# Optimization experiments

Measured on AMD Instinct MI355X. Metric: run time of the kernel, lower is better.

## Reference

```python
import jax, jax.numpy as jnp
import numpy as np
from jax import lax

B = 8; SEQ = 512; NVAR = 1024; PRED = 96; TFEAT = 7
DM = 128; DSTATE = 16; DCONV = 2; EL = 2; DFF = 128
DIN = DM                      # expand = 1
DTR = (DM + 15) // 16         # dt_rank = ceil(d_model/16) = 8


def setup_inputs() -> dict:
    key = jax.random.key(0)
    ks = iter(jax.random.split(key, 40))
    def rn(shape, s=0.02):
        return jax.random.normal(next(ks), shape, jnp.float32) * s
    inp = {}
    inp["x_enc"] = jax.random.normal(next(ks), (B, SEQ, NVAR), jnp.float32)
    inp["x_mark_enc"] = jax.random.normal(next(ks), (B, SEQ, TFEAT), jnp.float32)
    inp["x_dec"] = jnp.zeros((1, 1, 1), jnp.float32)
    inp["x_mark_dec"] = jnp.zeros((1, 1, 1), jnp.float32)
    # inverted embedding: Linear(seq_len -> d_model)
    inp["emb_w"] = rn((DM, SEQ)); inp["emb_b"] = jnp.zeros((DM,), jnp.float32)
    # Mamba params, stacked [e_layers, 2 directions, ...]
    inp["in_proj_w"] = rn((EL, 2, 2 * DIN, DM))
    inp["conv_w"] = rn((EL, 2, DIN, DCONV), 0.5)
    inp["conv_b"] = jnp.zeros((EL, 2, DIN), jnp.float32)
    inp["x_proj_w"] = rn((EL, 2, DTR + 2 * DSTATE, DIN))
    inp["dt_proj_w"] = rn((EL, 2, DIN, DTR), 0.5)
    inp["dt_proj_b"] = rn((EL, 2, DIN), 0.1)
    A_init = jnp.log(jnp.tile(jnp.arange(1, DSTATE + 1, dtype=jnp.float32), (DIN, 1)))
    inp["A_log"] = jnp.broadcast_to(A_init, (EL, 2, DIN, DSTATE)) * 1.0
    inp["D_param"] = jnp.ones((EL, 2, DIN), jnp.float32)
    inp["out_proj_w"] = rn((EL, 2, DM, DIN))
    # EncoderLayer norms + pointwise FFN (conv1/conv2 with kernel 1)
    inp["norm1_w"] = jnp.ones((EL, DM), jnp.float32); inp["norm1_b"] = jnp.zeros((EL, DM), jnp.float32)
    inp["norm2_w"] = jnp.ones((EL, DM), jnp.float32); inp["norm2_b"] = jnp.zeros((EL, DM), jnp.float32)
    inp["ffn_w1"] = rn((EL, DFF, DM)); inp["ffn_b1"] = jnp.zeros((EL, DFF), jnp.float32)
    inp["ffn_w2"] = rn((EL, DM, DFF)); inp["ffn_b2"] = jnp.zeros((EL, DM), jnp.float32)
    inp["fnorm_w"] = jnp.ones((DM,), jnp.float32); inp["fnorm_b"] = jnp.zeros((DM,), jnp.float32)
    inp["proj_w"] = rn((PRED, DM)); inp["proj_b"] = jnp.zeros((PRED,), jnp.float32)
    return inp


def _layernorm(x, w, b):
    mu = x.mean(-1, keepdims=True)
    var = ((x - mu) ** 2).mean(-1, keepdims=True)
    return (x - mu) / jnp.sqrt(var + 1e-5) * w + b


def _mamba(x, ipw, cw, cb, xpw, dpw, dpb, A_log, Dp, opw):
    # x: [B, L, DM]
    Bb, L, _ = x.shape
    xz = x @ ipw.T                                  # [B,L,2*DIN]
    xr, z = xz[..., :DIN], xz[..., DIN:]
    # causal depthwise conv1d, kernel DCONV, padding DCONV-1, truncated to L
    xp = jnp.pad(xr, ((0, 0), (DCONV - 1, 0), (0, 0)))
    xc = sum(xp[:, k:k + L, :] * cw[:, k] for k in range(DCONV)) + cb
    xc = jax.nn.silu(xc)
    dbc = xc @ xpw.T                                # [B,L,DTR+2*DSTATE]
    dt = dbc[..., :DTR]
    Bm = dbc[..., DTR:DTR + DSTATE]
    Cm = dbc[..., DTR + DSTATE:]
    delta = jax.nn.softplus(dt @ dpw.T + dpb)       # [B,L,DIN]
    A = -jnp.exp(A_log)                             # [DIN,DSTATE]
    dA = jnp.exp(delta[..., None] * A)              # [B,L,DIN,DSTATE]
    dBu = delta[..., None] * Bm[:, :, None, :] * xc[..., None]

    def step(h, t):
        dA_t, dBu_t, C_t = t
        h = dA_t * h + dBu_t                        # [B,DIN,DSTATE]
        y = jnp.einsum('bdn,bn->bd', h, C_t)
        return h, y

    h0 = jnp.zeros((Bb, DIN, DSTATE), x.dtype)
    _, ys = lax.scan(step, h0, (dA.transpose(1, 0, 2, 3), dBu.transpose(1, 0, 2, 3), Cm.transpose(1, 0, 2)))
    y = ys.transpose(1, 0, 2) + Dp * xc             # [B,L,DIN]
    y = y * jax.nn.silu(z)
    return y @ opw.T


def reference(x_enc, x_mark_enc, x_dec, x_mark_dec, emb_w, emb_b, in_proj_w, conv_w, conv_b,
              x_proj_w, dt_proj_w, dt_proj_b, A_log, D_param, out_proj_w,
              norm1_w, norm1_b, norm2_w, norm2_b, ffn_w1, ffn_b1, ffn_w2, ffn_b2,
              fnorm_w, fnorm_b, proj_w, proj_b):
    N = x_enc.shape[-1]
    x = jnp.where(x_enc == -9999.0, -1.0, x_enc)
    # inverted embedding: variate tokens + 7 time-feature tokens
    tokens = jnp.concatenate([x.transpose(0, 2, 1), x_mark_enc.transpose(0, 2, 1)], axis=1)  # [B,N+7,SEQ]
    h = tokens @ emb_w.T + emb_b                    # [B,N+7,DM]
    for l in range(EL):
        fwd = _mamba(h, in_proj_w[l, 0], conv_w[l, 0], conv_b[l, 0], x_proj_w[l, 0],
                     dt_proj_w[l, 0], dt_proj_b[l, 0], A_log[l, 0], D_param[l, 0], out_proj_w[l, 0])
        rev = _mamba(h[:, ::-1], in_proj_w[l, 1], conv_w[l, 1], conv_b[l, 1], x_proj_w[l, 1],
                     dt_proj_w[l, 1], dt_proj_b[l, 1], A_log[l, 1], D_param[l, 1], out_proj_w[l, 1])[:, ::-1]
        h = h + fwd + rev
        y = h = _layernorm(h, norm1_w[l], norm1_b[l])
        y = jax.nn.relu(y @ ffn_w1[l].T + ffn_b1[l])
        y = y @ ffn_w2[l].T + ffn_b2[l]
        h = _layernorm(h + y, norm2_w[l], norm2_b[l])
    h = _layernorm(h, fnorm_w, fnorm_b)
    dec = (h @ proj_w.T + proj_b).transpose(0, 2, 1)[:, :, :N]  # [B,PRED,N]
    return dec[:, -PRED:, :]
```

## Files before the change

kernel.cpp:

```cpp
#include <hip/hip_runtime.h>
#include <math.h>


#define L_SEQ 1031
#define LP    1088
#define TC    68
#define NCH   16
#define BATCH 8
#define NVAR  1024
#define SEQQ  512
#define TFEAT 7

#define SZ_H    ((size_t)BATCH * L_SEQ * 128)
#define SZ_XZ   ((size_t)2 * BATCH * L_SEQ * 256)
#define SZ_DT   ((size_t)2 * BATCH * 128 * LP)
#define SZ_BC   ((size_t)2 * BATCH * 16 * LP)
#define OFF_H    ((size_t)0)
#define OFF_H1   (OFF_H + SZ_H)
#define OFF_XZ   (OFF_H1 + SZ_H)
#define OFF_XCT  (OFF_XZ + SZ_XZ)
#define OFF_DLT  (OFF_XCT + SZ_DT)
#define OFF_BMT  (OFF_DLT + SZ_DT)
#define OFF_CMT  (OFF_BMT + SZ_BC)
#define OFF_YT   (OFF_CMT + SZ_BC)
#define SZ_SUM  ((size_t)2 * BATCH * NCH * 128 * 16)

typedef __bf16 bf16_t;
typedef bf16_t bf16x4 __attribute__((ext_vector_type(4)));
typedef bf16_t bf16x8 __attribute__((ext_vector_type(8)));
typedef float floatx4 __attribute__((ext_vector_type(4)));

#define MFMA16(a, b, c) __builtin_amdgcn_mfma_f32_16x16x32_bf16((a), (b), (c), 0, 0, 0)

__device__ __forceinline__ float silu_f(float x) {
  return x / (1.f + __expf(-x));
}
__device__ __forceinline__ float softplus_f(float x) {
  return (x > 20.f) ? x : log1pf(__expf(x));
}
__device__ __forceinline__ float red8(float x) {
  x += __int_as_float(__builtin_amdgcn_update_dpp(
      0, __float_as_int(x), 0xB1, 0xF, 0xF, true));
  x += __int_as_float(__builtin_amdgcn_update_dpp(
      0, __float_as_int(x), 0x4E, 0xF, 0xF, true));
  x += __int_as_float(__builtin_amdgcn_update_dpp(
      0, __float_as_int(x), 0x141, 0xF, 0xF, true));
  return x;
}


#define STAGE_W128(WBUF, SRC, LDK, K0)                                       \
  _Pragma("unroll")                                                          \
  for (int i_ = 0; i_ < 16; i_++) {                                          \
    int e_ = tid + i_ * 256;                                                 \
    int n_ = e_ >> 5, kq_ = e_ & 31;                                         \
    float4 wv_ = *(const float4*)&(SRC)[(size_t)n_ * (LDK) + (K0) + kq_ * 4];\
    bf16x4 bv_ = {(bf16_t)wv_.x, (bf16_t)wv_.y, (bf16_t)wv_.z, (bf16_t)wv_.w};\
    *(bf16x4*)&WBUF[n_][kq_ * 4] = bv_;                                      \
  }

#define MFMA_K128(ABUF, WBUF, ACC)                                           \
  _Pragma("unroll")                                                          \
  for (int kc_ = 0; kc_ < 4; kc_++) {                                        \
    bf16x8 a_ = *(const bf16x8*)&ABUF[arow][kc_ * 32 + q8];                  \
    _Pragma("unroll")                                                        \
    for (int nt_ = 0; nt_ < 4; nt_++) {                                      \
      bf16x8 b_ = *(const bf16x8*)&WBUF[wcol + nt_ * 16 + ln][kc_ * 32 + q8];\
      ACC[nt_] = MFMA16(a_, b_, ACC[nt_]);                                   \
    }                                                                        \
  }

__global__ __launch_bounds__(256) void k_embed(
    const float* __restrict__ x_enc, const float* __restrict__ x_mark,
    const float* __restrict__ emb_w, const float* __restrict__ emb_b,
    float* __restrict__ H) {
  int b = blockIdx.y;
  int v0 = blockIdx.x * 32;
  int tid = threadIdx.x;
  __shared__ bf16_t Abf[32][136];
  __shared__ bf16_t Wbf[128][136];
  int lane = tid & 63, ln = lane & 15, q = lane >> 4, q8 = q * 8;
  int w = tid >> 6, rw = w & 1, cw = w >> 1;
  int arow = rw * 16 + ln, wcol = cw * 64;
  floatx4 acc[4];
#pragma unroll
  for (int nt = 0; nt < 4; nt++) acc[nt] = (floatx4){0.f, 0.f, 0.f, 0.f};

  for (int c = 0; c < 4; c++) {
    int s0 = c * 128;
#pragma unroll
    for (int i = 0; i < 4; i++) {
      int e = tid + i * 256;
      int s = e >> 3, vq = e & 7;
      int vg = v0 + vq * 4;
      float4 xv;
      if (vg + 3 < NVAR) {
        xv = *(const float4*)&x_enc[((size_t)b * SEQQ + s0 + s) * NVAR + vg];
        if (xv.x == -9999.f) xv.x = -1.f;
        if (xv.y == -9999.f) xv.y = -1.f;
        if (xv.z == -9999.f) xv.z = -1.f;
        if (xv.w == -9999.f) xv.w = -1.f;
      } else {
        float tmp[4];
#pragma unroll
        for (int u = 0; u < 4; u++) {
          int v = vg + u;
          tmp[u] = (v < L_SEQ)
                       ? x_mark[((size_t)b * SEQQ + s0 + s) * TFEAT + (v - NVAR)]
                       : 0.f;
        }
        xv = make_float4(tmp[0], tmp[1], tmp[2], tmp[3]);
      }
      Abf[vq * 4 + 0][s] = (bf16_t)xv.x;
      Abf[vq * 4 + 1][s] = (bf16_t)xv.y;
      Abf[vq * 4 + 2][s] = (bf16_t)xv.z;
      Abf[vq * 4 + 3][s] = (bf16_t)xv.w;
    }
    STAGE_W128(Wbf, emb_w, SEQQ, s0);
    __syncthreads();
    MFMA_K128(Abf, Wbf, acc);
    __syncthreads();
  }
#pragma unroll
  for (int r = 0; r < 4; r++) {
    int v = v0 + rw * 16 + q * 4 + r;
    if (v < L_SEQ) {
      float* dst = &H[((size_t)b * L_SEQ + v) * 128];
#pragma unroll
      for (int nt = 0; nt < 4; nt++) {
        int col = wcol + nt * 16 + ln;
        dst[col] = acc[nt][r] + emb_b[col];
      }
    }
  }
}

__global__ __launch_bounds__(256) void k_xz(
    const float* __restrict__ H, const float* __restrict__ ipw,
    float* __restrict__ XZ, int l) {
  int b = blockIdx.y;
  int dir = blockIdx.z >> 1, nh = blockIdx.z & 1;
  int t0 = blockIdx.x * 32;
  int tid = threadIdx.x;
  __shared__ bf16_t Abf[32][136];
  __shared__ bf16_t Wbf[128][136];
  int lane = tid & 63, ln = lane & 15, q = lane >> 4, q8 = q * 8;
  int w = tid >> 6, rw = w & 1, cw = w >> 1;
  int arow = rw * 16 + ln, wcol = cw * 64;
  floatx4 acc[4];
#pragma unroll
  for (int nt = 0; nt < 4; nt++) acc[nt] = (floatx4){0.f, 0.f, 0.f, 0.f};
  const float* wbase = ipw + (size_t)(l * 2 + dir) * 256 * 128 + (size_t)nh * 128 * 128;

#pragma unroll
  for (int i = 0; i < 4; i++) {
    int e = tid + i * 256;
    int tl = e >> 5, kq = e & 31;
    int t = t0 + tl;
    float4 hv = make_float4(0.f, 0.f, 0.f, 0.f);
    if (t < L_SEQ) {
      int st = dir ? (L_SEQ - 1 - t) : t;
      hv = *(const float4*)&H[((size_t)b * L_SEQ + st) * 128 + kq * 4];
    }
    bf16x4 av = {(bf16_t)hv.x, (bf16_t)hv.y, (bf16_t)hv.z, (bf16_t)hv.w};
    *(bf16x4*)&Abf[tl][kq * 4] = av;
  }
  STAGE_W128(Wbf, wbase, 128, 0);
  __syncthreads();
  MFMA_K128(Abf, Wbf, acc);

#pragma unroll
  for (int r = 0; r < 4; r++) {
    int t = t0 + rw * 16 + q * 4 + r;
    if (t < L_SEQ) {
      float* dst = XZ + ((size_t)(dir * BATCH + b) * L_SEQ + t) * 256 + nh * 128;
#pragma unroll
      for (int nt = 0; nt < 4; nt++) dst[wcol + nt * 16 + ln] = acc[nt][r];
    }
  }
}

__global__ __launch_bounds__(256) void k_mid(
    const float* __restrict__ XZ,
    const float* __restrict__ conv_w, const float* __restrict__ conv_b,
    const float* __restrict__ xpw,
    const float* __restrict__ dpw, const float* __restrict__ dpb,
    float* __restrict__ XCT, float* __restrict__ DLT,
    float* __restrict__ BmT, float* __restrict__ CmT, int l) {
  int b = blockIdx.y, dir = blockIdx.z;
  int t0 = blockIdx.x * 32;
  int tid = threadIdx.x;
  int pg = l * 2 + dir;
  __shared__ float xcs[32][132];
  __shared__ float xpws[40][128];
  __shared__ float dbcs[40][36];
  const float* xz = XZ + (size_t)(dir * BATCH + b) * L_SEQ * 256;

  for (int i = 0; i < 20; i++) {
    int e = tid + i * 256;
    int k = e & 127, j = e >> 7;
    xpws[j][k] = xpw[((size_t)pg * 40 + j) * 128 + k];
  }
  for (int i = 0; i < 16; i++) {
    int e = tid + i * 256;
    int d = e & 127, tl = e >> 7;
    int t = t0 + tl;
    float v = 0.f;
    if (t < L_SEQ) {
      float x1 = xz[(size_t)t * 256 + d];
      float x0 = (t > 0) ? xz[(size_t)(t - 1) * 256 + d] : 0.f;
      float c0 = conv_w[((size_t)pg * 128 + d) * 2 + 0];
      float c1 = conv_w[((size_t)pg * 128 + d) * 2 + 1];
      v = silu_f(x0 * c0 + x1 * c1 + conv_b[(size_t)pg * 128 + d]);
    }
    xcs[tl][d] = v;
  }
  __syncthreads();
  {
    int tl = tid & 31, jg = tid >> 5;
    float acc[5] = {0.f};
    const float4* xrow = (const float4*)&xcs[tl][0];
    for (int kk = 0; kk < 32; kk++) {
      float4 a = xrow[kk];
#pragma unroll
      for (int jj = 0; jj < 5; jj++) {
        float4 w = ((const float4*)&xpws[jg * 5 + jj][0])[kk];
        acc[jj] = fmaf(a.x, w.x, acc[jj]);
        acc[jj] = fmaf(a.y, w.y, acc[jj]);
        acc[jj] = fmaf(a.z, w.z, acc[jj]);
        acc[jj] = fmaf(a.w, w.w, acc[jj]);
      }
    }
#pragma unroll
    for (int jj = 0; jj < 5; jj++) dbcs[jg * 5 + jj][tl] = acc[jj];
  }
  __syncthreads();
  for (int i = 0; i < 4; i++) {
    int e = tid + i * 256;
    int tl = e & 31, r = e >> 5;
    int n = r & 15, isC = r >> 4;
    int t = t0 + tl;
    if (t < LP) {
      float v = dbcs[8 + isC * 16 + n][tl];
      float* dst = isC ? CmT : BmT;
      dst[((size_t)(dir * BATCH + b) * 16 + n) * LP + t] = v;
    }
  }
  {
    int d = tid & 127, th = tid >> 7;
    float dw[8];
#pragma unroll
    for (int k = 0; k < 8; k++) dw[k] = dpw[((size_t)pg * 128 + d) * 8 + k];
    float dbv = dpb[(size_t)pg * 128 + d];
    size_t base = ((size_t)(dir * BATCH + b) * 128 + d) * LP;
    for (int tb = th * 16; tb < th * 16 + 16; tb += 4) {
      int t = t0 + tb;
      if (t < LP) {
        float dv[4], xv[4];
#pragma unroll
        for (int u = 0; u < 4; u++) {
          int tl = tb + u;
          float a = dbv;
#pragma unroll
          for (int k = 0; k < 8; k++) a = fmaf(dbcs[k][tl], dw[k], a);
          dv[u] = softplus_f(a);
          xv[u] = xcs[tl][d];
        }
        *(float4*)(DLT + base + t) = make_float4(dv[0], dv[1], dv[2], dv[3]);
        *(float4*)(XCT + base + t) = make_float4(xv[0], xv[1], xv[2], xv[3]);
      }
    }
  }
}

__global__ __launch_bounds__(64) void k_scan1(
    const float* __restrict__ DLT, const float* __restrict__ XCT,
    const float* __restrict__ BmT,
    const float* __restrict__ A_log,
    float* __restrict__ sumH, float* __restrict__ sumP, int l) {
  int z = blockIdx.z;
  int dir = z >> 4, j = z & 15;
  int b = blockIdx.y;
  int lane = threadIdx.x;
  int np = lane & 7, ds = lane >> 3;
  int d = blockIdx.x * 8 + ds;
  int pg = l * 2 + dir;
  int n0 = np * 2;
  float A0 = -__expf(A_log[((size_t)pg * 128 + d) * 16 + n0]);
  float A1 = -__expf(A_log[((size_t)pg * 128 + d) * 16 + n0 + 1]);
  size_t bd = ((size_t)(dir * BATCH + b) * 128 + d) * LP + (size_t)j * TC;
  size_t bn = ((size_t)(dir * BATCH + b) * 16 + n0) * LP + (size_t)j * TC;
  const float4* dl4 = (const float4*)(DLT + bd);
  const float4* xc4 = (const float4*)(XCT + bd);
  const float4* b04 = (const float4*)(BmT + bn);
  const float4* b14 = (const float4*)(BmT + bn + LP);
  float h0 = 0.f, h1 = 0.f, sdl = 0.f;
  const int NI = TC / 4;
  float4 cd = dl4[0], cx = xc4[0], cb0 = b04[0], cb1 = b14[0];
#define P1STEP(DL, XC, B0, B1)                       \
  {                                                  \
    float du_ = (DL) * (XC);                         \
    h0 = fmaf(__expf((DL) * A0), h0, du_ * (B0));    \
    h1 = fmaf(__expf((DL) * A1), h1, du_ * (B1));    \
  }
  for (int i = 0; i < NI; i++) {
    float4 nd = cd, nx = cx, nb0 = cb0, nb1 = cb1;
    if (i + 1 < NI) {
      nd = dl4[i + 1]; nx = xc4[i + 1];
      nb0 = b04[i + 1]; nb1 = b14[i + 1];
    }
    P1STEP(cd.x, cx.x, cb0.x, cb1.x);
    P1STEP(cd.y, cx.y, cb0.y, cb1.y);
    P1STEP(cd.z, cx.z, cb0.z, cb1.z);
    P1STEP(cd.w, cx.w, cb0.w, cb1.w);
    sdl += (cd.x + cd.y) + (cd.z + cd.w);
    cd = nd; cx = nx; cb0 = nb0; cb1 = nb1;
  }
#undef P1STEP
  size_t si = (((size_t)(dir * BATCH + b) * NCH + j) * 128 + d) * 16 + n0;
  *(float2*)&sumH[si] = make_float2(h0, h1);
  *(float2*)&sumP[si] = make_float2(__expf(A0 * sdl), __expf(A1 * sdl));
}

__global__ __launch_bounds__(64) void k_scan2(
    const float* __restrict__ DLT, const float* __restrict__ XCT,
    const float* __restrict__ BmT, const float* __restrict__ CmT,
    const float* __restrict__ XZ,
    const float* __restrict__ A_log, const float* __restrict__ Dpar,
    const float* __restrict__ sumH, const float* __restrict__ sumP,
    float* __restrict__ YT, int l) {
  int z = blockIdx.z;
  int dir = z >> 4, j = z & 15;
  int b = blockIdx.y;
  int lane = threadIdx.x;
  int np = lane & 7, ds = lane >> 3;
  int d = blockIdx.x * 8 + ds;
  int pg = l * 2 + dir;
  int n0 = np * 2;
  float A0 = -__expf(A_log[((size_t)pg * 128 + d) * 16 + n0]);
  float A1 = -__expf(A_log[((size_t)pg * 128 + d) * 16 + n0 + 1]);
  float Dv = Dpar[(size_t)pg * 128 + d];
  float h0 = 0.f, h1 = 0.f;
  {
    size_t sbase = ((size_t)(dir * BATCH + b) * NCH) * 2048 + (size_t)d * 16 + n0;
    for (int jj = 0; jj < j; jj++) {
      float2 hE = *(const float2*)&sumH[sbase + (size_t)jj * 2048];
      float2 Pp = *(const float2*)&sumP[sbase + (size_t)jj * 2048];
      h0 = fmaf(Pp.x, h0, hE.x);
      h1 = fmaf(Pp.y, h1, hE.y);
    }
  }
  size_t bd = ((size_t)(dir * BATCH + b) * 128 + d) * LP + (size_t)j * TC;
  size_t bn = ((size_t)(dir * BATCH + b) * 16 + n0) * LP + (size_t)j * TC;
  const float4* dl4 = (const float4*)(DLT + bd);
  const float4* xc4 = (const float4*)(XCT + bd);
  const float4* b04 = (const float4*)(BmT + bn);
  const float4* b14 = (const float4*)(BmT + bn + LP);
  const float4* c04 = (const float4*)(CmT + bn);
  const float4* c14 = (const float4*)(CmT + bn + LP);
  const float* zbase = XZ + (size_t)(dir * BATCH + b) * L_SEQ * 256 + 128 + d
                       + (size_t)j * TC * 256;
  float* ybase = YT + ((size_t)(dir * BATCH + b) * LP + (size_t)j * TC) * 128 + d;
  const int NI = TC / 4;
  float4 cd = dl4[0], cx = xc4[0], cb0 = b04[0], cb1 = b14[0];
  float4 cc0 = c04[0], cc1 = c14[0];
  float zc[4], zn[4];
  if (np == 0) {
#pragma unroll
    for (int u = 0; u < 4; u++) zc[u] = zbase[(size_t)u * 256];
  }
#define STEP1(DL, XC, B0, B1, C0, C1, YO)            \
  {                                                  \
    float du_ = (DL) * (XC);                         \
    h0 = fmaf(__expf((DL) * A0), h0, du_ * (B0));    \
    h1 = fmaf(__expf((DL) * A1), h1, du_ * (B1));    \
    float p_ = red8(fmaf(h1, (C1), h0 * (C0)));      \
    (YO) = fmaf(Dv, (XC), p_);                       \
  }
  for (int i = 0; i < NI; i++) {
    float4 nd = cd, nx = cx, nb0 = cb0, nb1 = cb1, nc0 = cc0, nc1 = cc1;
    if (i + 1 < NI) {
      nd = dl4[i + 1]; nx = xc4[i + 1];
      nb0 = b04[i + 1]; nb1 = b14[i + 1];
      nc0 = c04[i + 1]; nc1 = c14[i + 1];
      if (np == 0) {
        int tb = (i + 1) * 4;
#pragma unroll
        for (int u = 0; u < 4; u++) zn[u] = zbase[(size_t)(tb + u) * 256];
      }
    }
    float4 y;
    STEP1(cd.x, cx.x, cb0.x, cb1.x, cc0.x, cc1.x, y.x);
    STEP1(cd.y, cx.y, cb0.y, cb1.y, cc0.y, cc1.y, y.y);
    STEP1(cd.z, cx.z, cb0.z, cb1.z, cc0.z, cc1.z, y.z);
    STEP1(cd.w, cx.w, cb0.w, cb1.w, cc0.w, cc1.w, y.w);
    if (np == 0) {
      y.x *= silu_f(zc[0]);
      y.y *= silu_f(zc[1]);
      y.z *= silu_f(zc[2]);
      y.w *= silu_f(zc[3]);
      int tb = i * 4;
      ybase[(size_t)(tb + 0) * 128] = y.x;
      ybase[(size_t)(tb + 1) * 128] = y.y;
      ybase[(size_t)(tb + 2) * 128] = y.z;
      ybase[(size_t)(tb + 3) * 128] = y.w;
#pragma unroll
      for (int u = 0; u < 4; u++) zc[u] = zn[u];
    }
    cd = nd; cx = nx; cb0 = nb0; cb1 = nb1; cc0 = nc0; cc1 = nc1;
  }
#undef STEP1
}

__global__ __launch_bounds__(256) void k_out(
    const float* __restrict__ YT, const float* __restrict__ Hin,
    const float* __restrict__ opw,
    const float* __restrict__ n1w, const float* __restrict__ n1b,
    float* __restrict__ H1, int l) {
  int b = blockIdx.y;
  int t0 = blockIdx.x * 32;
  int tid = threadIdx.x;
  __shared__ bf16_t Abf[32][136];
  __shared__ bf16_t Wbf[128][136];
  __shared__ float Ssum[2][32][2];
  int lane = tid & 63, ln = lane & 15, q = lane >> 4, q8 = q * 8;
  int w = tid >> 6, rw = w & 1, cw = w >> 1;
  int arow = rw * 16 + ln, wcol = cw * 64;
  floatx4 acc[4];
#pragma unroll
  for (int nt = 0; nt < 4; nt++) acc[nt] = (floatx4){0.f, 0.f, 0.f, 0.f};

  for (int dirp = 0; dirp < 2; dirp++) {
    const float* ysrc = YT + (size_t)(dirp * BATCH + b) * LP * 128;
#pragma unroll
    for (int i = 0; i < 4; i++) {
      int e = tid + i * 256;
      int tl = e >> 5, dq = e & 31;
      int tg = t0 + tl;
      int srow = dirp ? (L_SEQ - 1 - tg) : tg;
      float4 yv = make_float4(0.f, 0.f, 0.f, 0.f);
      if (srow >= 0) yv = *(const float4*)&ysrc[(size_t)srow * 128 + dq * 4];
      bf16x4 av = {(bf16_t)yv.x, (bf16_t)yv.y, (bf16_t)yv.z, (bf16_t)yv.w};
      *(bf16x4*)&Abf[tl][dq * 4] = av;
    }
    const float* wsrc = opw + (size_t)(l * 2 + dirp) * 128 * 128;
    STAGE_W128(Wbf, wsrc, 128, 0);
    __syncthreads();
    MFMA_K128(Abf, Wbf, acc);
    __syncthreads();
  }
  const float* nw = n1w + l * 128;
  const float* nbv = n1b + l * 128;
  float vres[4][4];
  float s1r[4], s2r[4];
#pragma unroll
  for (int r = 0; r < 4; r++) {
    int t = t0 + rw * 16 + q * 4 + r;
    float s1 = 0.f, s2 = 0.f;
#pragma unroll
    for (int nt = 0; nt < 4; nt++) {
      int col = wcol + nt * 16 + ln;
      float resid = (t < L_SEQ) ? Hin[((size_t)b * L_SEQ + t) * 128 + col] : 0.f;
      float v = acc[nt][r] + resid;
      vres[r][nt] = v;
      s1 += v;
      s2 += v * v;
    }
#pragma unroll
    for (int m = 1; m < 16; m <<= 1) {
      s1 += __shfl_xor(s1, m);
      s2 += __shfl_xor(s2, m);
    }
    s1r[r] = s1; s2r[r] = s2;
  }
  if (ln == 0) {
#pragma unroll
    for (int r = 0; r < 4; r++) {
      Ssum[cw][rw * 16 + q * 4 + r][0] = s1r[r];
      Ssum[cw][rw * 16 + q * 4 + r][1] = s2r[r];
    }
  }
  __syncthreads();
#pragma unroll
  for (int r = 0; r < 4; r++) {
    int row = rw * 16 + q * 4 + r;
    float s1 = s1r[r] + Ssum[cw ^ 1][row][0];
    float s2 = s2r[r] + Ssum[cw ^ 1][row][1];
    float mean = s1 * (1.f / 128.f);
    float rstd = rsqrtf(s2 * (1.f / 128.f) - mean * mean + 1e-5f);
    int t = t0 + row;
    if (t < L_SEQ) {
#pragma unroll
      for (int nt = 0; nt < 4; nt++) {
        int col = wcol + nt * 16 + ln;
        H1[((size_t)b * L_SEQ + t) * 128 + col] =
            (vres[r][nt] - mean) * rstd * nw[col] + nbv[col];
      }
    }
  }
}

__global__ __launch_bounds__(256) void k_ffn(
    const float* __restrict__ H1, const float* __restrict__ w1,
    const float* __restrict__ b1, const float* __restrict__ w2,
    const float* __restrict__ b2, const float* __restrict__ n2w,
    const float* __restrict__ n2b, float* __restrict__ Hout, int l) {
  int b = blockIdx.y;
  int t0 = blockIdx.x * 32;
  int tid = threadIdx.x;
  __shared__ bf16_t Abf[32][136];
  __shared__ bf16_t Wbf[128][136];
  __shared__ bf16_t Ut[32][136];
  __shared__ float Ssum[2][32][2];
  int lane = tid & 63, ln = lane & 15, q = lane >> 4, q8 = q * 8;
  int w = tid >> 6, rw = w & 1, cw = w >> 1;
  int arow = rw * 16 + ln, wcol = cw * 64;
  floatx4 acc[4];
#pragma unroll
  for (int nt = 0; nt < 4; nt++) acc[nt] = (floatx4){0.f, 0.f, 0.f, 0.f};
  const float* w1b = w1 + (size_t)l * 128 * 128;
  const float* w2b = w2 + (size_t)l * 128 * 128;

#pragma unroll
  for (int i = 0; i < 4; i++) {
    int e = tid + i * 256;
    int tl = e >> 5, kq = e & 31;
    int t = t0 + tl;
    float4 hv = make_float4(0.f, 0.f, 0.f, 0.f);
    if (t < L_SEQ)
      hv = *(const float4*)&H1[((size_t)b * L_SEQ + t) * 128 + kq * 4];
    bf16x4 av = {(bf16_t)hv.x, (bf16_t)hv.y, (bf16_t)hv.z, (bf16_t)hv.w};
    *(bf16x4*)&Abf[tl][kq * 4] = av;
  }
  STAGE_W128(Wbf, w1b, 128, 0);
  __syncthreads();
  MFMA_K128(Abf, Wbf, acc);
  __syncthreads();
  {
    float b1v[4];
#pragma unroll
    for (int nt = 0; nt < 4; nt++) b1v[nt] = b1[l * 128 + wcol + nt * 16 + ln];
#pragma unroll
    for (int nt = 0; nt < 4; nt++) {
#pragma unroll
      for (int r = 0; r < 4; r++) {
        Ut[rw * 16 + q * 4 + r][wcol + nt * 16 + ln] =
            (bf16_t)fmaxf(acc[nt][r] + b1v[nt], 0.f);
      }
      acc[nt] = (floatx4){0.f, 0.f, 0.f, 0.f};
    }
  }
  STAGE_W128(Wbf, w2b, 128, 0);
  __syncthreads();
  MFMA_K128(Ut, Wbf, acc);
  const float* nw = n2w + l * 128;
  const float* nbv = n2b + l * 128;
  float vres[4][4];
  float s1r[4], s2r[4];
#pragma unroll
  for (int r = 0; r < 4; r++) {
    int t = t0 + rw * 16 + q * 4 + r;
    float s1 = 0.f, s2 = 0.f;
#pragma unroll
    for (int nt = 0; nt < 4; nt++) {
      int col = wcol + nt * 16 + ln;
      float resid = (t < L_SEQ) ? H1[((size_t)b * L_SEQ + t) * 128 + col] : 0.f;
      float v = acc[nt][r] + b2[l * 128 + col] + resid;
      vres[r][nt] = v;
      s1 += v;
      s2 += v * v;
    }
#pragma unroll
    for (int m = 1; m < 16; m <<= 1) {
      s1 += __shfl_xor(s1, m);
      s2 += __shfl_xor(s2, m);
    }
    s1r[r] = s1; s2r[r] = s2;
  }
  __syncthreads();
  if (ln == 0) {
#pragma unroll
    for (int r = 0; r < 4; r++) {
      Ssum[cw][rw * 16 + q * 4 + r][0] = s1r[r];
      Ssum[cw][rw * 16 + q * 4 + r][1] = s2r[r];
    }
  }
  __syncthreads();
#pragma unroll
  for (int r = 0; r < 4; r++) {
    int row = rw * 16 + q * 4 + r;
    float s1 = s1r[r] + Ssum[cw ^ 1][row][0];
    float s2 = s2r[r] + Ssum[cw ^ 1][row][1];
    float mean = s1 * (1.f / 128.f);
    float rstd = rsqrtf(s2 * (1.f / 128.f) - mean * mean + 1e-5f);
    int t = t0 + row;
    if (t < L_SEQ) {
#pragma unroll
      for (int nt = 0; nt < 4; nt++) {
        int col = wcol + nt * 16 + ln;
        Hout[((size_t)b * L_SEQ + t) * 128 + col] =
            (vres[r][nt] - mean) * rstd * nw[col] + nbv[col];
      }
    }
  }
}

__global__ __launch_bounds__(256) void k_final(
    const float* __restrict__ Hsrc, const float* __restrict__ fw,
    const float* __restrict__ fb, const float* __restrict__ pw,
    const float* __restrict__ pb, float* __restrict__ out) {
  int b = blockIdx.y;
  int v0 = blockIdx.x * 16;
  int tid = threadIdx.x;
  __shared__ float At[128][17];
  __shared__ float Ws[32][97];
  __shared__ float Os[96][17];
  for (int i = 0; i < 8; i++) {
    int e = tid + i * 256;
    int k = e & 127, tl = e >> 7;
    At[k][tl] = Hsrc[((size_t)b * L_SEQ + v0 + tl) * 128 + k];
  }
  __syncthreads();
  {
    int g = tid & 15, tl = tid >> 4;
    float s1 = 0.f, s2 = 0.f;
#pragma unroll
    for (int kk = 0; kk < 8; kk++) {
      float v = At[g * 8 + kk][tl];
      s1 += v;
      s2 += v * v;
    }
#pragma unroll
    for (int msk = 1; msk < 16; msk <<= 1) {
      s1 += __shfl_xor(s1, msk);
      s2 += __shfl_xor(s2, msk);
    }
    float mean = s1 * (1.f / 128.f);
    float rstd = rsqrtf(s2 * (1.f / 128.f) - mean * mean + 1e-5f);
#pragma unroll
    for (int kk = 0; kk < 8; kk++) {
      int k = g * 8 + kk;
      At[k][tl] = (At[k][tl] - mean) * rstd * fw[k] + fb[k];
    }
  }
  __syncthreads();
  int tm = tid & 15, tt = tid >> 4;
  float acc[6] = {0.f};
  for (int k0 = 0; k0 < 128; k0 += 32) {
    for (int i = 0; i < 12; i++) {
      int e = tid + i * 256;
      int ki = e & 31, p = e >> 5;
      Ws[ki][p] = pw[(size_t)p * 128 + k0 + ki];
    }
    __syncthreads();
    for (int ki = 0; ki < 32; ki++) {
      float a = At[k0 + ki][tt];
#pragma unroll
      for (int jq = 0; jq < 6; jq++)
        acc[jq] = fmaf(a, Ws[ki][tm + jq * 16], acc[jq]);
    }
    __syncthreads();
  }
#pragma unroll
  for (int jq = 0; jq < 6; jq++) {
    int p = tm + jq * 16;
    Os[p][tt] = acc[jq] + pb[p];
  }
  __syncthreads();
  for (int i = 0; i < 6; i++) {
    int e = tid + i * 256;
    int vi = e & 15, p = e >> 4;
    out[((size_t)b * 96 + p) * 1024 + v0 + vi] = Os[p][vi];
  }
}

extern "C" void kernel_launch(void* const* d_in, const int* in_sizes, int n_in,
                              void* d_out, int out_size, void* d_ws, size_t ws_size,
                              hipStream_t stream) {
  (void)in_sizes; (void)n_in; (void)out_size; (void)ws_size;
  const float* x_enc  = (const float*)d_in[0];
  const float* x_mark = (const float*)d_in[1];
  const float* emb_w  = (const float*)d_in[4];
  const float* emb_b  = (const float*)d_in[5];
  const float* ipw    = (const float*)d_in[6];
  const float* cw     = (const float*)d_in[7];
  const float* cb     = (const float*)d_in[8];
  const float* xpw    = (const float*)d_in[9];
  const float* dpw    = (const float*)d_in[10];
  const float* dpb    = (const float*)d_in[11];
  const float* A_log  = (const float*)d_in[12];
  const float* Dpar   = (const float*)d_in[13];
  const float* opw    = (const float*)d_in[14];
  const float* n1w    = (const float*)d_in[15];
  const float* n1b    = (const float*)d_in[16];
  const float* n2w    = (const float*)d_in[17];
  const float* n2b    = (const float*)d_in[18];
  const float* fw1    = (const float*)d_in[19];
  const float* fb1    = (const float*)d_in[20];
  const float* fw2    = (const float*)d_in[21];
  const float* fb2    = (const float*)d_in[22];
  const float* fnw    = (const float*)d_in[23];
  const float* fnb    = (const float*)d_in[24];
  const float* pw     = (const float*)d_in[25];
  const float* pb     = (const float*)d_in[26];

  float* ws   = (float*)d_ws;
  float* H    = ws + OFF_H;
  float* H1   = ws + OFF_H1;
  float* XZ   = ws + OFF_XZ;
  float* XCT  = ws + OFF_XCT;
  float* DLT  = ws + OFF_DLT;
  float* BmT  = ws + OFF_BMT;
  float* CmT  = ws + OFF_CMT;
  float* YT   = ws + OFF_YT;
  float* sumH = ws + OFF_H1;
  float* sumP = ws + OFF_H1 + SZ_SUM;

  k_embed<<<dim3(33, 8), 256, 0, stream>>>(x_enc, x_mark, emb_w, emb_b, H);
  for (int l = 0; l < 2; l++) {
    k_xz<<<dim3(33, 8, 4), 256, 0, stream>>>(H, ipw, XZ, l);
    k_mid<<<dim3(34, 8, 2), 256, 0, stream>>>(XZ, cw, cb, xpw, dpw, dpb,
                                              XCT, DLT, BmT, CmT, l);
    k_scan1<<<dim3(16, 8, 32), 64, 0, stream>>>(DLT, XCT, BmT, A_log,
                                                sumH, sumP, l);
    k_scan2<<<dim3(16, 8, 32), 64, 0, stream>>>(DLT, XCT, BmT, CmT, XZ,
                                                A_log, Dpar, sumH, sumP, YT, l);
    k_out<<<dim3(33, 8), 256, 0, stream>>>(YT, H, opw, n1w, n1b, H1, l);
    k_ffn<<<dim3(33, 8), 256, 0, stream>>>(H1, fw1, fb1, fw2, fb2, n2w, n2b, H, l);
  }
  k_final<<<dim3(64, 8), 256, 0, stream>>>(H, fnw, fnb, pw, pb, (float*)d_out);
}
```

Baseline: 399.2 us.

## Split selective scan into 32 shorter chunks and store chunk delta sums compactly

Result: slower. 417.5 us (+4.6%).

```diff
diff --git a/kernel.cpp b/kernel.cpp
--- a/kernel.cpp
+++ b/kernel.cpp
@@ -3,9 +3,10 @@
 
 
 #define L_SEQ 1031
-#define LP    1088
-#define TC    68
-#define NCH   16
+#define LP    1152
+#define TC    36
+#define NCH   32
+#define SDROW 1056
 #define BATCH 8
 #define NVAR  1024
 #define SEQQ  512
@@ -47,7 +48,6 @@
       0, __float_as_int(x), 0x141, 0xF, 0xF, true));
   return x;
 }
-
 
 #define STAGE_W128(WBUF, SRC, LDK, K0)                                       \
   _Pragma("unroll")                                                          \
@@ -277,19 +277,20 @@
     const float* __restrict__ DLT, const float* __restrict__ XCT,
     const float* __restrict__ BmT,
     const float* __restrict__ A_log,
-    float* __restrict__ sumH, float* __restrict__ sumP, int l) {
+    float* __restrict__ sumH, float* __restrict__ YT, int l) {
   int z = blockIdx.z;
-  int dir = z >> 4, j = z & 15;
+  int dir = z >> 5, j = z & 31;
   int b = blockIdx.y;
   int lane = threadIdx.x;
   int np = lane & 7, ds = lane >> 3;
   int d = blockIdx.x * 8 + ds;
   int pg = l * 2 + dir;
   int n0 = np * 2;
+  int dirb = dir * BATCH + b;
   float A0 = -__expf(A_log[((size_t)pg * 128 + d) * 16 + n0]);
   float A1 = -__expf(A_log[((size_t)pg * 128 + d) * 16 + n0 + 1]);
-  size_t bd = ((size_t)(dir * BATCH + b) * 128 + d) * LP + (size_t)j * TC;
-  size_t bn = ((size_t)(dir * BATCH + b) * 16 + n0) * LP + (size_t)j * TC;
+  size_t bd = ((size_t)dirb * 128 + d) * LP + (size_t)j * TC;
+  size_t bn = ((size_t)dirb * 16 + n0) * LP + (size_t)j * TC;
   const float4* dl4 = (const float4*)(DLT + bd);
   const float4* xc4 = (const float4*)(XCT + bd);
   const float4* b04 = (const float4*)(BmT + bn);
@@ -317,9 +318,11 @@
     cd = nd; cx = nx; cb0 = nb0; cb1 = nb1;
   }
 #undef P1STEP
-  size_t si = (((size_t)(dir * BATCH + b) * NCH + j) * 128 + d) * 16 + n0;
+  size_t si = (((size_t)dirb * NCH + j) * 128 + d) * 16 + n0;
   *(float2*)&sumH[si] = make_float2(h0, h1);
-  *(float2*)&sumP[si] = make_float2(__expf(A0 * sdl), __expf(A1 * sdl));
+  if (np == 0) {
+    YT[((size_t)dirb * LP + SDROW + j) * 128 + d] = sdl;
+  }
 }
 
 __global__ __launch_bounds__(64) void k_scan2(
@@ -327,40 +330,42 @@
     const float* __restrict__ BmT, const float* __restrict__ CmT,
     const float* __restrict__ XZ,
     const float* __restrict__ A_log, const float* __restrict__ Dpar,
-    const float* __restrict__ sumH, const float* __restrict__ sumP,
+    const float* __restrict__ sumH,
     float* __restrict__ YT, int l) {
   int z = blockIdx.z;
-  int dir = z >> 4, j = z & 15;
+  int dir = z >> 5, j = z & 31;
   int b = blockIdx.y;
   int lane = threadIdx.x;
   int np = lane & 7, ds = lane >> 3;
   int d = blockIdx.x * 8 + ds;
   int pg = l * 2 + dir;
   int n0 = np * 2;
+  int dirb = dir * BATCH + b;
   float A0 = -__expf(A_log[((size_t)pg * 128 + d) * 16 + n0]);
   float A1 = -__expf(A_log[((size_t)pg * 128 + d) * 16 + n0 + 1]);
   float Dv = Dpar[(size_t)pg * 128 + d];
   float h0 = 0.f, h1 = 0.f;
   {
-    size_t sbase = ((size_t)(dir * BATCH + b) * NCH) * 2048 + (size_t)d * 16 + n0;
+    size_t sbase = ((size_t)dirb * NCH) * 2048 + (size_t)d * 16 + n0;
+    const float* sdbase = YT + ((size_t)dirb * LP + SDROW) * 128 + d;
     for (int jj = 0; jj < j; jj++) {
       float2 hE = *(const float2*)&sumH[sbase + (size_t)jj * 2048];
-      float2 Pp = *(const float2*)&sumP[sbase + (size_t)jj * 2048];
-      h0 = fmaf(Pp.x, h0, hE.x);
-      h1 = fmaf(Pp.y, h1, hE.y);
-    }
-  }
-  size_t bd = ((size_t)(dir * BATCH + b) * 128 + d) * LP + (size_t)j * TC;
-  size_t bn = ((size_t)(dir * BATCH + b) * 16 + n0) * LP + (size_t)j * TC;
+      float sdl = sdbase[(size_t)jj * 128];
+      h0 = fmaf(__expf(A0 * sdl), h0, hE.x);
+      h1 = fmaf(__expf(A1 * sdl), h1, hE.y);
+    }
+  }
+  size_t bd = ((size_t)dirb * 128 + d) * LP + (size_t)j * TC;
+  size_t bn = ((size_t)dirb * 16 + n0) * LP + (size_t)j * TC;
   const float4* dl4 = (const float4*)(DLT + bd);
   const float4* xc4 = (const float4*)(XCT + bd);
   const float4* b04 = (const float4*)(BmT + bn);
   const float4* b14 = (const float4*)(BmT + bn + LP);
   const float4* c04 = (const float4*)(CmT + bn);
   const float4* c14 = (const float4*)(CmT + bn + LP);
-  const float* zbase = XZ + (size_t)(dir * BATCH + b) * L_SEQ * 256 + 128 + d
+  const float* zbase = XZ + (size_t)dirb * L_SEQ * 256 + 128 + d
                        + (size_t)j * TC * 256;
-  float* ybase = YT + ((size_t)(dir * BATCH + b) * LP + (size_t)j * TC) * 128 + d;
+  float* ybase = YT + ((size_t)dirb * LP + (size_t)j * TC) * 128 + d;
   const int NI = TC / 4;
   float4 cd = dl4[0], cx = xc4[0], cb0 = b04[0], cb1 = b14[0];
   float4 cc0 = c04[0], cc1 = c14[0];
@@ -395,15 +400,13 @@
     STEP1(cd.z, cx.z, cb0.z, cb1.z, cc0.z, cc1.z, y.z);
     STEP1(cd.w, cx.w, cb0.w, cb1.w, cc0.w, cc1.w, y.w);
     if (np == 0) {
-      y.x *= silu_f(zc[0]);
-      y.y *= silu_f(zc[1]);
-      y.z *= silu_f(zc[2]);
-      y.w *= silu_f(zc[3]);
-      int tb = i * 4;
-      ybase[(size_t)(tb + 0) * 128] = y.x;
-      ybase[(size_t)(tb + 1) * 128] = y.y;
-      ybase[(size_t)(tb + 2) * 128] = y.z;
-      ybase[(size_t)(tb + 3) * 128] = y.w;
+      int tg = j * TC + i * 4;
+      float yv[4] = {y.x * silu_f(zc[0]), y.y * silu_f(zc[1]),
+                     y.z * silu_f(zc[2]), y.w * silu_f(zc[3])};
+#pragma unroll
+      for (int u = 0; u < 4; u++) {
+        if (tg + u < SDROW) ybase[(size_t)(i * 4 + u) * 128] = yv[u];
+      }
 #pragma unroll
       for (int u = 0; u < 4; u++) zc[u] = zn[u];
     }
@@ -714,17 +717,16 @@
   float* CmT  = ws + OFF_CMT;
   float* YT   = ws + OFF_YT;
   float* sumH = ws + OFF_H1;
-  float* sumP = ws + OFF_H1 + SZ_SUM;
 
   k_embed<<<dim3(33, 8), 256, 0, stream>>>(x_enc, x_mark, emb_w, emb_b, H);
   for (int l = 0; l < 2; l++) {
     k_xz<<<dim3(33, 8, 4), 256, 0, stream>>>(H, ipw, XZ, l);
-    k_mid<<<dim3(34, 8, 2), 256, 0, stream>>>(XZ, cw, cb, xpw, dpw, dpb,
+    k_mid<<<dim3(36, 8, 2), 256, 0, stream>>>(XZ, cw, cb, xpw, dpw, dpb,
                                               XCT, DLT, BmT, CmT, l);
-    k_scan1<<<dim3(16, 8, 32), 64, 0, stream>>>(DLT, XCT, BmT, A_log,
-                                                sumH, sumP, l);
-    k_scan2<<<dim3(16, 8, 32), 64, 0, stream>>>(DLT, XCT, BmT, CmT, XZ,
-                                                A_log, Dpar, sumH, sumP, YT, l);
+    k_scan1<<<dim3(16, 8, 64), 64, 0, stream>>>(DLT, XCT, BmT, A_log,
+                                                sumH, YT, l);
+    k_scan2<<<dim3(16, 8, 64), 64, 0, stream>>>(DLT, XCT, BmT, CmT, XZ,
+                                                A_log, Dpar, sumH, YT, l);
     k_out<<<dim3(33, 8), 256, 0, stream>>>(YT, H, opw, n1w, n1b, H1, l);
     k_ffn<<<dim3(33, 8), 256, 0, stream>>>(H1, fw1, fb1, fw2, fb2, n2w, n2b, H, l);
   }
```
